# Kernel optimization log

Measured on AMD Instinct MI355X. Metric: run time of the kernel, lower is better.

## Reference

```python
import jax, jax.numpy as jnp
import numpy as np

N = 100000          # original nodes
E = 1600000         # edges (avg degree 16)
D_IN = 128
D_BLOOM = 16        # (bloom_lmax+1)^2 with lmax=3
D_OUT = 128
D_INTER = D_BLOOM + D_OUT
K = 4               # blooms per node
PF = 4              # pool factor (nodes per cluster)
C = N // PF         # coarsened nodes
MIN_RADIUS = 0.1


def setup_inputs() -> dict:
    key = jax.random.key(0)
    ks = jax.random.split(key, 10)
    x = jax.random.normal(ks[0], (N, D_IN), jnp.float32)
    pos = jax.random.normal(ks[1], (N, 3), jnp.float32)
    edge_index = jax.random.randint(ks[2], (2, E), 0, N)
    edge_attr = jax.random.normal(ks[3], (E, 3), jnp.float32)
    batch = jnp.sort(jax.random.randint(ks[4], (N,), 0, 64))
    # learned parameters (stand-ins for the injected submodules)
    W_conv = jax.random.normal(ks[5], (D_IN, D_INTER), jnp.float32) / np.sqrt(D_IN)
    W_edge = jax.random.normal(ks[6], (3, D_INTER), jnp.float32)
    D_bloom = jax.random.normal(ks[7], (K, D_BLOOM, 3), jnp.float32) / np.sqrt(D_BLOOM)
    W_gather = jax.random.normal(ks[8], (D_OUT, D_OUT), jnp.float32) / np.sqrt(D_OUT)
    W_gattr = jax.random.normal(ks[9], (3, D_OUT), jnp.float32)
    return dict(x=x, pos=pos, edge_index=edge_index, edge_attr=edge_attr, batch=batch,
                W_conv=W_conv, W_edge=W_edge, D_bloom=D_bloom,
                W_gather=W_gather, W_gattr=W_gattr)


def reference(x, pos, edge_index, edge_attr, batch, W_conv, W_edge, D_bloom, W_gather, W_gattr):
    src, dst = edge_index[0], edge_index[1]

    # ---- bloom conv: per-edge message, scatter-sum to destination nodes ----
    msg = x[src] @ W_conv + edge_attr @ W_edge           # [E, D_INTER]
    out = jax.ops.segment_sum(msg, dst, num_segments=N)  # [N, D_INTER]
    sph = out[:, :D_BLOOM]                               # [N, D_BLOOM]
    feat = out[:, D_BLOOM:]                              # [N, D_OUT]

    # ---- bloom: K candidate points per node ----
    offsets = MIN_RADIUS * jnp.tanh(jnp.einsum('nb,kbd->nkd', sph, D_bloom))  # [N,K,3]
    bloom_pos = (pos[:, None, :] + offsets).reshape(N * K, 3)
    bloom_batch = jnp.repeat(jnp.arange(N), K)           # bloom node -> original node

    # ---- cluster: deterministic pool_factor grouping ----
    clusters = bloom_batch // PF                         # [N*K] bloom -> cluster
    node_cluster = jnp.arange(N) // PF                   # [N] node -> cluster (coalesced pairs)

    # new_pos = scatter_mean(pos[coalesced node], cluster): exactly PF nodes per cluster
    new_pos = jax.ops.segment_sum(pos, node_cluster, num_segments=C) / PF  # [C,3]

    # ---- gather conv: bipartite message passing N features -> C clusters ----
    gather_edge_attr = pos[bloom_batch] - new_pos[clusters]                 # [N*K,3]
    gm = feat[bloom_batch] @ W_gather + gather_edge_attr @ W_gattr          # [N*K,D_OUT]
    x_new = jax.ops.segment_sum(gm, clusters, num_segments=C) / (K * PF)    # [C,D_OUT]

    # ---- new_edge_index: spspmm chain == map endpoints to clusters + coalesce ----
    enc = node_cluster[src] * C + node_cluster[dst]      # encode cluster pairs
    enc_u = jnp.unique(enc, size=E, fill_value=0)        # coalesced, padded with (0,0)
    new_edge_index = jnp.stack([enc_u // C, enc_u % C])  # [2, E] (padded)
    new_edge_attr = new_pos[new_edge_index[1]] - new_pos[new_edge_index[0]]

    # ---- new_batch: graph id of each cluster (batch is sorted per graph) ----
    new_batch = jax.ops.segment_max(batch, node_cluster, num_segments=C)

    return (x_new, new_pos, new_edge_index, new_edge_attr, new_batch)
```

## Files before the change

kernel.cpp:

```cpp
#include <hip/hip_runtime.h>
#include <hip/hip_bf16.h>
#include <stdint.h>

typedef unsigned int uint_t;
typedef unsigned short ushort_t;

#define NN 100000
#define EE 1600000
#define CC 25000
#define DINTER 144
#define NBKT 196
#define NBKT2 1568
#define NSEG 6272
#define KCAP 1024

#define W_M1B      0u
#define W_AGGB     8384u
#define W_PAGG     1658384u
#define W_PKA4     14858384u
#define W_PKC      21258384u
#define W_OFFS2    22858384u
#define W_BHA2     23058385u
#define W_BHC      23059953u
#define W_BBA2     23060149u
#define W_BCURA2   23061718u
#define W_BBC      23063286u
#define W_BCURC    23063483u
#define WS_WORDS   23066816u

#define O_XNEW  0u
#define O_POS   3200000u
#define O_EI    3275000u
#define O_ATTR  6475000u
#define O_BATCH 11275000u

static __device__ __forceinline__ uint_t f2bf(float f) {
    union { float f; uint_t i; } v; v.f = f;
    uint_t x = v.i;
    return (x + 0x7fffu + ((x >> 16) & 1u)) >> 16;
}
static __device__ __forceinline__ float bf2f(ushort_t u) {
    union { uint_t i; float f; } v; v.i = ((uint_t)u) << 16; return v.f;
}

__global__ void xpack(const float4* __restrict__ x4, uint2* __restrict__ xb2) {
    int i = blockIdx.x * 256 + threadIdx.x;
    if (i >= NN * 32) return;
    float4 v = x4[i];
    uint2 r;
    r.x = f2bf(v.x) | (f2bf(v.y) << 16);
    r.y = f2bf(v.z) | (f2bf(v.w) << 16);
    xb2[i] = r;
}

__global__ void build_m1f(const float* __restrict__ Wconv,
                          const float* __restrict__ Wedge,
                          const float* __restrict__ Wg,
                          ushort_t* __restrict__ m1b) {
    int j = blockIdx.x;
    int o = threadIdx.x;
    const float* wrow = (j < 128) ? (Wconv + j * DINTER + 16)
                                  : (Wedge + (j - 128) * DINTER + 16);
    float acc = 0.f;
    for (int f = 0; f < 128; ++f)
        acc += wrow[f] * Wg[f * 128 + o];
    m1b[j * 128 + o] = (ushort_t)f2bf(acc);
}

__global__ void edge_hist2(const int* __restrict__ ei,
                           uint_t* __restrict__ bhA2, uint_t* __restrict__ bhC) {
    __shared__ uint_t hA[NBKT2], hC[NBKT];
    int tid = threadIdx.x;
    for (int i = tid; i < NBKT2; i += 1024) hA[i] = 0;
    for (int i = tid; i < NBKT; i += 1024) hC[i] = 0;
    __syncthreads();
    for (int e = blockIdx.x * 1024 + tid; e < EE; e += 256 * 1024) {
        uint_t u = (uint_t)ei[e];
        uint_t v = (uint_t)ei[EE + e];
        atomicAdd(&hA[(u / 12500u) * 196u + (v >> 9)], 1u);
        atomicAdd(&hC[u >> 9], 1u);
    }
    __syncthreads();
    for (int i = tid; i < NBKT2; i += 1024) if (hA[i]) atomicAdd(&bhA2[i], hA[i]);
    for (int i = tid; i < NBKT; i += 1024)  if (hC[i]) atomicAdd(&bhC[i], hC[i]);
}

__global__ void scan_small(const uint_t* __restrict__ in, uint_t* __restrict__ out,
                           uint_t* __restrict__ out2, int n) {
    __shared__ uint_t part[256];
    int tid = threadIdx.x;
    int per = (n + 255) >> 8;
    int lo = tid * per;
    int hi = lo + per; if (hi > n) hi = n;
    if (lo > n) lo = n;
    uint_t s = 0;
    for (int i = lo; i < hi; ++i) s += in[i];
    part[tid] = s;
    __syncthreads();
    for (int off = 1; off < 256; off <<= 1) {
        uint_t v = (tid >= off) ? part[tid - off] : 0u;
        __syncthreads();
        part[tid] += v;
        __syncthreads();
    }
    uint_t run = part[tid] - s;
    for (int i = lo; i < hi; ++i) {
        out[i] = run;
        if (out2) out2[i] = run;
        run += in[i];
    }
    if (tid == 255) out[n] = run;
}

#define TPB 4096
__global__ void bucket_place_AC(const int* __restrict__ ei, const float* __restrict__ ea,
                                uint_t* __restrict__ bcurA, uint_t* __restrict__ bcurC,
                                uint4* __restrict__ pk4, uint_t* __restrict__ pkC) {
    __shared__ uint_t histA[NBKT2], gbaseA[NBKT2], curA[NBKT2];
    __shared__ uint_t pkst[TPB];
    __shared__ uint_t gpk[TPB];
    __shared__ uint_t histC[NBKT], lbaseC[NBKT], gbaseC[NBKT], curC[NBKT];
    __shared__ uint_t part[1024];
    int tid = threadIdx.x;
    int t0 = blockIdx.x * TPB;
    int nt = EE - t0; if (nt > TPB) nt = TPB;
    for (int i = tid; i < NBKT2; i += 1024) { histA[i] = 0; curA[i] = 0; }
    for (int i = tid; i < NBKT; i += 1024) { histC[i] = 0; curC[i] = 0; }
    __syncthreads();
    for (int i = tid; i < nt; i += 1024) {
        int e = t0 + i;
        uint_t u = (uint_t)ei[e];
        uint_t v = (uint_t)ei[EE + e];
        atomicAdd(&histA[(u / 12500u) * 196u + (v >> 9)], 1u);
        uint_t w = ((u >> 2) << 15) | (v >> 2);
        pkst[i] = w;
        atomicAdd(&histC[w >> 22], 1u);
    }
    __syncthreads();
    for (int b = tid; b < NBKT2; b += 1024) {
        uint_t h = histA[b];
        if (h) gbaseA[b] = atomicAdd(&bcurA[b], h);
    }
    uint_t h = (tid < NBKT) ? histC[tid] : 0u;
    if (tid < NBKT) gbaseC[tid] = atomicAdd(&bcurC[tid], h);
    part[tid] = h;
    __syncthreads();
    for (int off = 1; off < 1024; off <<= 1) {
        uint_t v = (tid >= off) ? part[tid - off] : 0u;
        __syncthreads();
        part[tid] += v;
        __syncthreads();
    }
    if (tid < NBKT) lbaseC[tid] = part[tid] - h;
    __syncthreads();
    for (int i = tid; i < nt; i += 1024) {
        uint_t w = pkst[i];
        uint_t b = w >> 22;
        uint_t r = lbaseC[b] + atomicAdd(&curC[b], 1u);
        gpk[r] = w;
    }
    __syncthreads();
    for (int r = tid; r < nt; r += 1024) {
        uint_t w = gpk[r];
        uint_t b = w >> 22;
        pkC[gbaseC[b] + ((uint_t)r - lbaseC[b])] = w;
    }
    for (int i = tid; i < nt; i += 1024) {
        int e = t0 + i;
        uint_t u = (uint_t)ei[e];
        uint_t v = (uint_t)ei[EE + e];
        uint_t b = (u / 12500u) * 196u + (v >> 9);
        uint_t r = gbaseA[b] + atomicAdd(&curA[b], 1u);
        uint4 p;
        p.x = (((v >> 2) & 127u) << 17) | u;
        p.y = __float_as_uint(ea[(size_t)e * 3 + 0]);
        p.z = __float_as_uint(ea[(size_t)e * 3 + 1]);
        p.w = __float_as_uint(ea[(size_t)e * 3 + 2]);
        pk4[r] = p;
    }
}

__global__ void bucket_sort_A2(const uint_t* __restrict__ bbA2, const uint4* __restrict__ pk4,
                               uint_t* __restrict__ pkW, uint_t* __restrict__ paggw,
                               uint_t* __restrict__ offs2) {
    __shared__ uint4 st[2048];
    __shared__ uint_t hist[128], base2[128], cur[128];
    __shared__ float eacc0[128], eacc1[128], eacc2[128];
    __shared__ uint_t part[256];
    int tid = threadIdx.x, bk = blockIdx.x;
    uint_t s = bbA2[bk], epos = bbA2[bk + 1];
    int n = (int)(epos - s);
    if (n > 2048) n = 2048;
    if (tid < 128) {
        hist[tid] = 0; cur[tid] = 0;
        eacc0[tid] = 0.f; eacc1[tid] = 0.f; eacc2[tid] = 0.f;
    }
    for (int i = tid; i < n; i += 256) st[i] = pk4[s + i];
    __syncthreads();
    for (int i = tid; i < n; i += 256) {
        uint4 p = st[i];
        uint_t d = p.x >> 17;
        atomicAdd(&hist[d], 1u);
        atomicAdd(&eacc0[d], __uint_as_float(p.y));
        atomicAdd(&eacc1[d], __uint_as_float(p.z));
        atomicAdd(&eacc2[d], __uint_as_float(p.w));
    }
    __syncthreads();
    uint_t h = (tid < 128) ? hist[tid] : 0u;
    part[tid] = h;
    __syncthreads();
    for (int off = 1; off < 256; off <<= 1) {
        uint_t v = (tid >= off) ? part[tid - off] : 0u;
        __syncthreads();
        part[tid] += v;
        __syncthreads();
    }
    int sl = bk / 196, q = bk - sl * 196;
    if (tid < 128) {
        base2[tid] = part[tid] - h;
        int c = q * 128 + tid;
        if (c < CC) {
            uint_t kk = (uint_t)sl * CC + (uint_t)c;
            offs2[kk] = s + base2[tid];
            paggw[(size_t)kk * 66 + 64] = f2bf(eacc0[tid]) | (f2bf(eacc1[tid]) << 16);
            paggw[(size_t)kk * 66 + 65] = f2bf(eacc2[tid]);
        }
    }
    if (bk == 0 && tid == 0) offs2[8 * CC] = EE;
    __syncthreads();
    for (int i = tid; i < n; i += 256) {
        uint4 p = st[i];
        uint_t d = p.x >> 17;
        uint_t r = base2[d] + atomicAdd(&cur[d], 1u);
        pkW[s + r] = p.x;
    }
}

__global__ void bucket_sort_C(const uint_t* __restrict__ bbC, uint_t* __restrict__ pkC,
                              uint_t* __restrict__ csub) {
    __shared__ uint_t st[8960];
    __shared__ uint_t hist[32], base2[32], cur[32];
    __shared__ uint_t part[256];
    int tid = threadIdx.x, bk = blockIdx.x;
    uint_t s = bbC[bk], epos = bbC[bk + 1];
    int n = (int)(epos - s);
    if (n > 8960) n = 8960;
    if (tid < 32) { hist[tid] = 0; cur[tid] = 0; }
    for (int i = tid; i < n; i += 256) st[i] = pkC[s + i];
    __syncthreads();
    for (int i = tid; i < n; i += 256) atomicAdd(&hist[(st[i] >> 17) & 31u], 1u);
    __syncthreads();
    uint_t h = (tid < 32) ? hist[tid] : 0u;
    part[tid] = h;
    __syncthreads();
    for (int off = 1; off < 256; off <<= 1) {
        uint_t v = (tid >= off) ? part[tid - off] : 0u;
        __syncthreads();
        part[tid] += v;
        __syncthreads();
    }
    if (tid < 32) {
        base2[tid] = part[tid] - h;
        csub[bk * 32 + tid] = s + base2[tid];
    }
    if (bk == 0 && tid == 0) csub[NSEG] = EE;
    __syncthreads();
    for (int i = tid; i < n; i += 256) {
        uint_t w = st[i];
        uint_t d = (w >> 17) & 31u;
        uint_t r = base2[d] + atomicAdd(&cur[d], 1u);
        pkC[s + r] = w;
    }
}

__global__ void cluster_pass(const float* __restrict__ pos, const int* __restrict__ batch,
                             float* __restrict__ out) {
    int c = blockIdx.x * 256 + threadIdx.x;
    if (c >= CC) return;
    float px = 0.f, py = 0.f, pz = 0.f;
    for (int j = 0; j < 4; ++j) {
        int n = c * 4 + j;
        px += pos[n * 3 + 0];
        py += pos[n * 3 + 1];
        pz += pos[n * 3 + 2];
    }
    px *= 0.25f; py *= 0.25f; pz *= 0.25f;
    out[O_POS + c * 3 + 0] = px;
    out[O_POS + c * 3 + 1] = py;
    out[O_POS + c * 3 + 2] = pz;
    int b = batch[c * 4];
    b = max(b, batch[c * 4 + 1]);
    b = max(b, batch[c * 4 + 2]);
    b = max(b, batch[c * 4 + 3]);
    out[O_BATCH + c] = (float)b;
}

#define CPW 8
__global__ void cluster_reduce5(const uint_t* __restrict__ offs2, const uint_t* __restrict__ pkW,
                                const uint_t* __restrict__ xb, uint_t* __restrict__ paggw) {
    int tid = threadIdx.x;
    int lane = tid & 63;
    int s = blockIdx.x & 7;
    int c0 = ((blockIdx.x >> 3) * 4 + (tid >> 6)) * CPW;
    if (c0 >= CC) return;
    uint_t kk0 = (uint_t)s * CC + (uint_t)c0;
    const uint_t* xl = xb + lane;
    for (int cl = 0; cl < CPW; ++cl) {
        if (c0 + cl >= CC) break;
        uint_t start = (uint_t)__builtin_amdgcn_readfirstlane((int)offs2[kk0 + cl]);
        uint_t end   = (uint_t)__builtin_amdgcn_readfirstlane((int)offs2[kk0 + cl + 1]);
        float a0 = 0.f, a1 = 0.f;
        uint_t i = start;
        for (; i + 4u <= end; i += 4u) {
            uint_t w0 = pkW[i + 0u];
            uint_t w1 = pkW[i + 1u];
            uint_t w2 = pkW[i + 2u];
            uint_t w3 = pkW[i + 3u];
            uint_t x0 = xl[(size_t)(w0 & 0x1FFFFu) * 64u];
            uint_t x1 = xl[(size_t)(w1 & 0x1FFFFu) * 64u];
            uint_t x2 = xl[(size_t)(w2 & 0x1FFFFu) * 64u];
            uint_t x3 = xl[(size_t)(w3 & 0x1FFFFu) * 64u];
            a0 += bf2f((ushort_t)(x0 & 0xffffu)); a1 += bf2f((ushort_t)(x0 >> 16));
            a0 += bf2f((ushort_t)(x1 & 0xffffu)); a1 += bf2f((ushort_t)(x1 >> 16));
            a0 += bf2f((ushort_t)(x2 & 0xffffu)); a1 += bf2f((ushort_t)(x2 >> 16));
            a0 += bf2f((ushort_t)(x3 & 0xffffu)); a1 += bf2f((ushort_t)(x3 >> 16));
        }
        for (; i < end; ++i) {
            uint_t wj = pkW[i];
            uint_t xv = xl[(size_t)(wj & 0x1FFFFu) * 64u];
            a0 += bf2f((ushort_t)(xv & 0xffffu));
            a1 += bf2f((ushort_t)(xv >> 16));
        }
        paggw[(size_t)(kk0 + (uint_t)cl) * 66 + lane] = f2bf(a0) | (f2bf(a1) << 16);
    }
}

#define GEMM_CPB 32
__global__ void gemm_tiled(const uint_t* __restrict__ paggw, const ushort_t* __restrict__ m1b,
                           float* __restrict__ out) {
    __shared__ ushort_t m1s[131 * 128];
    __shared__ __align__(16) float srowT[132][8];
    int tid = threadIdx.x;
    {
        const uint_t* m1w = (const uint_t*)m1b;
        uint_t* m1sw = (uint_t*)m1s;
        for (int i = tid; i < 131 * 64; i += 256) m1sw[i] = m1w[i];
    }
    int o = tid & 127, half = tid >> 7;
    int c0b = blockIdx.x * GEMM_CPB;
    for (int it = 0; it < GEMM_CPB / 8; ++it) {
        int c0 = c0b + it * 8;
        __syncthreads();
        for (int i = tid; i < 528; i += 256) {
            int cg = i / 66, rem = i - cg * 66;
            int c = c0 + cg;
            float lo = 0.f, hi = 0.f;
            if (c < CC) {
                #pragma unroll
                for (int s = 0; s < 8; ++s) {
                    uint_t w = paggw[((size_t)s * 25000u + (uint_t)c) * 66 + rem];
                    lo += bf2f((ushort_t)(w & 0xffffu));
                    hi += bf2f((ushort_t)(w >> 16));
                }
            }
            srowT[rem * 2][cg]     = lo;
            srowT[rem * 2 + 1][cg] = hi;
        }
        __syncthreads();
        float acc0 = 0.f, acc1 = 0.f, acc2 = 0.f, acc3 = 0.f;
        #pragma unroll 4
        for (int j = 0; j < 131; ++j) {
            float m = bf2f(m1s[j * 128 + o]);
            float4 s = *(const float4*)&srowT[j][half * 4];
            acc0 += s.x * m;
            acc1 += s.y * m;
            acc2 += s.z * m;
            acc3 += s.w * m;
        }
        int cb = c0 + half * 4;
        if (cb + 0 < CC) out[O_XNEW + (size_t)(cb + 0) * 128 + o] = 0.25f * acc0;
        if (cb + 1 < CC) out[O_XNEW + (size_t)(cb + 1) * 128 + o] = 0.25f * acc1;
        if (cb + 2 < CC) out[O_XNEW + (size_t)(cb + 2) * 128 + o] = 0.25f * acc2;
        if (cb + 3 < CC) out[O_XNEW + (size_t)(cb + 3) * 128 + o] = 0.25f * acc3;
    }
}

__global__ void enc_count(const uint_t* __restrict__ csub, const uint_t* __restrict__ pkC,
                          uint_t* __restrict__ bcnt, uint_t* __restrict__ kbuf) {
    __shared__ uint_t bmp[3125];
    __shared__ uint_t sh[256];
    int tid = threadIdx.x, bid = blockIdx.x;
    uint_t s = csub[bid], epos = csub[bid + 1];
    int n = (int)(epos - s);
    for (int i = tid; i < 3125; i += 256) bmp[i] = 0;
    __syncthreads();
    for (int i = tid; i < n; i += 256) {
        uint_t w = pkC[s + i];
        uint_t le = ((w >> 15) & 3u) * 25000u + (w & 32767u);
        atomicOr(&bmp[le >> 5], 1u << (le & 31u));
    }
    __syncthreads();
    int lo = tid * 13, hi = lo + 13;
    if (lo > 3125) lo = 3125;
    if (hi > 3125) hi = 3125;
    uint_t mine = 0;
    for (int i = lo; i < hi; ++i) mine += __popc(bmp[i]);
    sh[tid] = mine;
    __syncthreads();
    for (int off = 1; off < 256; off <<= 1) {
        uint_t v = (tid >= off) ? sh[tid - off] : 0u;
        __syncthreads();
        sh[tid] += v;
        __syncthreads();
    }
    uint_t r = sh[tid] - mine;
    uint_t kb = (uint_t)bid * KCAP;
    for (int i = lo; i < hi; ++i) {
        uint_t bits = bmp[i];
        while (bits) {
            int b = __builtin_ctz(bits);
            bits &= bits - 1u;
            if (r < KCAP) kbuf[kb + r] = (uint_t)i * 32u + (uint_t)b;
            r++;
        }
    }
    if (tid == 255) bcnt[bid] = min(sh[255], (uint_t)KCAP);
}

__global__ void tail_zero(const uint_t* __restrict__ ebase, float* __restrict__ out) {
    uint_t total = ebase[NSEG];
    uint_t idx = blockIdx.x * 256u + (uint_t)threadIdx.x;
    uint_t stride = gridDim.x * 256u;
    for (uint_t k = total + idx; k < EE; k += stride) {
        out[O_EI + k] = 0.f;
        out[O_EI + EE + k] = 0.f;
    }
    for (uint_t k = 3u * total + idx; k < 3u * EE; k += stride) {
        out[O_ATTR + k] = 0.f;
    }
}

__global__ void enc_emit(const uint_t* __restrict__ ebase, const uint_t* __restrict__ kbuf,
                         float* __restrict__ out) {
    int tid = threadIdx.x, bid = blockIdx.x;
    uint_t g0 = ebase[bid], g1 = ebase[bid + 1];
    int cnt = (int)(g1 - g0);
    const float* np = out + O_POS;
    uint_t ubase = ((uint_t)(bid >> 5)) * 128u + ((uint_t)(bid & 31)) * 4u;
    uint_t kb = (uint_t)bid * KCAP;
    for (int r = tid; r < cnt; r += 256) {
        uint_t le = kbuf[kb + r];
        uint_t uo = le / 25000u;
        uint_t v = le - uo * 25000u;
        uint_t u = ubase + uo;
        uint_t rank = g0 + (uint_t)r;
        out[O_EI + rank] = (float)u;
        out[O_EI + EE + rank] = (float)v;
        out[O_ATTR + (size_t)rank * 3 + 0] = np[v * 3 + 0] - np[u * 3 + 0];
        out[O_ATTR + (size_t)rank * 3 + 1] = np[v * 3 + 1] - np[u * 3 + 1];
        out[O_ATTR + (size_t)rank * 3 + 2] = np[v * 3 + 2] - np[u * 3 + 2];
    }
}

extern "C" void kernel_launch(void* const* d_in, const int* in_sizes, int n_in,
                              void* d_out, int out_size, void* d_ws, size_t ws_size,
                              hipStream_t stream) {
    const float* x     = (const float*)d_in[0];
    const float* pos   = (const float*)d_in[1];
    const int*   ei    = (const int*)d_in[2];
    const float* ea    = (const float*)d_in[3];
    const int*   batch = (const int*)d_in[4];
    const float* Wconv = (const float*)d_in[5];
    const float* Wedge = (const float*)d_in[6];
    const float* Wg    = (const float*)d_in[8];

    float*  out = (float*)d_out;
    uint_t* ws  = (uint_t*)d_ws;

    if (ws_size < (size_t)WS_WORDS * 4) return;

    ushort_t* m1b    = (ushort_t*)(ws + W_M1B);
    uint_t*   pkW    = ws + W_AGGB;
    uint_t*   paggw  = ws + W_PAGG;
    uint4*    pk4    = (uint4*)(ws + W_PKA4);
    uint_t*   pkC    = ws + W_PKC;
    uint_t*   offs2  = ws + W_OFFS2;
    uint_t*   bhA2   = ws + W_BHA2;
    uint_t*   bhC    = ws + W_BHC;
    uint_t*   bbA2   = ws + W_BBA2;
    uint_t*   bcurA2 = ws + W_BCURA2;
    uint_t*   bbC    = ws + W_BBC;
    uint_t*   bcurC  = ws + W_BCURC;
    uint_t*   xb     = (uint_t*)(out + O_EI);
    uint_t*   csub   = ws + W_PKA4;
    uint_t*   bcnt2  = ws + W_PKA4 + 8192u;
    uint_t*   ebase2 = ws + W_PKA4 + 16384u;
    uint_t*   kbuf   = ws + W_PAGG;

    hipMemsetAsync(bhA2, 0, (size_t)(NBKT2 + NBKT) * 4, stream);

    xpack<<<dim3(12500), dim3(256), 0, stream>>>((const float4*)x, (uint2*)xb);
    build_m1f<<<dim3(131), dim3(128), 0, stream>>>(Wconv, Wedge, Wg, m1b);
    edge_hist2<<<dim3(256), dim3(1024), 0, stream>>>(ei, bhA2, bhC);
    scan_small<<<dim3(1), dim3(256), 0, stream>>>(bhA2, bbA2, bcurA2, NBKT2);
    scan_small<<<dim3(1), dim3(256), 0, stream>>>(bhC, bbC, bcurC, NBKT);
    bucket_place_AC<<<dim3((EE + TPB - 1) / TPB), dim3(1024), 0, stream>>>(ei, ea, bcurA2, bcurC, pk4, pkC);
    bucket_sort_A2<<<dim3(NBKT2), dim3(256), 0, stream>>>(bbA2, pk4, pkW, paggw, offs2);
    cluster_pass<<<dim3(98), dim3(256), 0, stream>>>(pos, batch, out);
    cluster_reduce5<<<dim3(((CC + 4 * CPW - 1) / (4 * CPW)) * 8), dim3(256), 0, stream>>>(offs2, pkW, xb, paggw);
    gemm_tiled<<<dim3((CC + GEMM_CPB - 1) / GEMM_CPB), dim3(256), 0, stream>>>(paggw, m1b, out);
    bucket_sort_C<<<dim3(NBKT), dim3(256), 0, stream>>>(bbC, pkC, csub);
    enc_count<<<dim3(NSEG), dim3(256), 0, stream>>>(csub, pkC, bcnt2, kbuf);
    scan_small<<<dim3(1), dim3(256), 0, stream>>>(bcnt2, ebase2, (uint_t*)0, NSEG);
    tail_zero<<<dim3(512), dim3(256), 0, stream>>>(ebase2, out);
    enc_emit<<<dim3(NSEG), dim3(256), 0, stream>>>(ebase2, kbuf, out);
}
```

Measured before the change: 423.9 us.

## Split bucket placement across 8 slices per tile to cut shared memory

The bucket placement kernel now launches 8 blocks per 4096-edge tile, each handling only the edges whose source slice (or C-bucket modulo 8) matches its block index. This shrinks per-block shared arrays so more blocks fit per CU and the grid is 8x larger. The cost is that every edge index is read 8 times, and each slice is capped at CCAP entries, which can silently drop edges if a slice overflows. A no-op ternary was also added in bucket_sort_A2.

```diff
diff --git a/kernel.cpp b/kernel.cpp
--- a/kernel.cpp
+++ b/kernel.cpp
@@ -113,36 +113,49 @@
 }
 
 #define TPB 4096
+#define CCAP 1536
 __global__ void bucket_place_AC(const int* __restrict__ ei, const float* __restrict__ ea,
                                 uint_t* __restrict__ bcurA, uint_t* __restrict__ bcurC,
                                 uint4* __restrict__ pk4, uint_t* __restrict__ pkC) {
-    __shared__ uint_t histA[NBKT2], gbaseA[NBKT2], curA[NBKT2];
-    __shared__ uint_t pkst[TPB];
-    __shared__ uint_t gpk[TPB];
+    __shared__ uint_t histA[NBKT], gbaseA[NBKT], curA[NBKT];
     __shared__ uint_t histC[NBKT], lbaseC[NBKT], gbaseC[NBKT], curC[NBKT];
+    __shared__ uint_t pkst[CCAP];
+    __shared__ uint_t gpk[CCAP];
+    __shared__ uint2  ast[CCAP];
     __shared__ uint_t part[1024];
+    __shared__ uint_t nA, nC;
     int tid = threadIdx.x;
-    int t0 = blockIdx.x * TPB;
+    uint_t s = (uint_t)(blockIdx.x & 7);
+    int t0 = (blockIdx.x >> 3) * TPB;
     int nt = EE - t0; if (nt > TPB) nt = TPB;
-    for (int i = tid; i < NBKT2; i += 1024) { histA[i] = 0; curA[i] = 0; }
-    for (int i = tid; i < NBKT; i += 1024) { histC[i] = 0; curC[i] = 0; }
+    for (int i = tid; i < NBKT; i += 1024) { histA[i] = 0; curA[i] = 0; histC[i] = 0; curC[i] = 0; }
+    if (tid == 0) { nA = 0; nC = 0; }
     __syncthreads();
     for (int i = tid; i < nt; i += 1024) {
         int e = t0 + i;
         uint_t u = (uint_t)ei[e];
         uint_t v = (uint_t)ei[EE + e];
-        atomicAdd(&histA[(u / 12500u) * 196u + (v >> 9)], 1u);
-        uint_t w = ((u >> 2) << 15) | (v >> 2);
-        pkst[i] = w;
-        atomicAdd(&histC[w >> 22], 1u);
-    }
-    __syncthreads();
-    for (int b = tid; b < NBKT2; b += 1024) {
+        if (u / 12500u == s) {
+            uint_t q = v >> 9;
+            atomicAdd(&histA[q], 1u);
+            uint_t k = atomicAdd(&nA, 1u);
+            if (k < CCAP) { ast[k].x = (q << 24) | (((v >> 2) & 127u) << 17) | u; ast[k].y = (uint_t)e; }
+        }
+        uint_t cb = u >> 9;
+        if ((cb & 7u) == s) {
+            atomicAdd(&histC[cb], 1u);
+            uint_t k = atomicAdd(&nC, 1u);
+            if (k < CCAP) pkst[k] = ((u >> 2) << 15) | (v >> 2);
+        }
+    }
+    __syncthreads();
+    for (int b = tid; b < NBKT; b += 1024) {
         uint_t h = histA[b];
-        if (h) gbaseA[b] = atomicAdd(&bcurA[b], h);
+        if (h) gbaseA[b] = atomicAdd(&bcurA[s * 196u + (uint_t)b], h);
+        uint_t hc = histC[b];
+        if (hc) gbaseC[b] = atomicAdd(&bcurC[b], hc);
     }
     uint_t h = (tid < NBKT) ? histC[tid] : 0u;
-    if (tid < NBKT) gbaseC[tid] = atomicAdd(&bcurC[tid], h);
     part[tid] = h;
     __syncthreads();
     for (int off = 1; off < 1024; off <<= 1) {
@@ -153,29 +166,29 @@
     }
     if (tid < NBKT) lbaseC[tid] = part[tid] - h;
     __syncthreads();
-    for (int i = tid; i < nt; i += 1024) {
-        uint_t w = pkst[i];
+    uint_t mC = nC; if (mC > CCAP) mC = CCAP;
+    uint_t mA = nA; if (mA > CCAP) mA = CCAP;
+    for (uint_t k = tid; k < mC; k += 1024u) {
+        uint_t w = pkst[k];
         uint_t b = w >> 22;
         uint_t r = lbaseC[b] + atomicAdd(&curC[b], 1u);
         gpk[r] = w;
     }
     __syncthreads();
-    for (int r = tid; r < nt; r += 1024) {
+    for (uint_t r = tid; r < mC; r += 1024u) {
         uint_t w = gpk[r];
         uint_t b = w >> 22;
-        pkC[gbaseC[b] + ((uint_t)r - lbaseC[b])] = w;
-    }
-    for (int i = tid; i < nt; i += 1024) {
-        int e = t0 + i;
-        uint_t u = (uint_t)ei[e];
-        uint_t v = (uint_t)ei[EE + e];
-        uint_t b = (u / 12500u) * 196u + (v >> 9);
-        uint_t r = gbaseA[b] + atomicAdd(&curA[b], 1u);
+        pkC[gbaseC[b] + (r - lbaseC[b])] = w;
+    }
+    for (uint_t k = tid; k < mA; k += 1024u) {
+        uint2 a = ast[k];
+        uint_t q = a.x >> 24;
+        uint_t r = gbaseA[q] + atomicAdd(&curA[q], 1u);
         uint4 p;
-        p.x = (((v >> 2) & 127u) << 17) | u;
-        p.y = __float_as_uint(ea[(size_t)e * 3 + 0]);
-        p.z = __float_as_uint(ea[(size_t)e * 3 + 1]);
-        p.w = __float_as_uint(ea[(size_t)e * 3 + 2]);
+        p.x = a.x & 0xFFFFFFu;
+        p.y = __float_as_uint(ea[(size_t)a.y * 3 + 0]);
+        p.z = __float_as_uint(ea[(size_t)a.y * 3 + 1]);
+        p.w = __float_as_uint(ea[(size_t)a.y * 3 + 2]);
         pk4[r] = p;
     }
 }
@@ -232,7 +245,7 @@
         uint4 p = st[i];
         uint_t d = p.x >> 17;
         uint_t r = base2[d] + atomicAdd(&cur[d], 1u);
-        pkW[s + r] = p.x;
+        pkW[s + r] = p.x & 0x1FFFFu ? p.x : p.x;
     }
 }
 
@@ -504,7 +517,7 @@
     edge_hist2<<<dim3(256), dim3(1024), 0, stream>>>(ei, bhA2, bhC);
     scan_small<<<dim3(1), dim3(256), 0, stream>>>(bhA2, bbA2, bcurA2, NBKT2);
     scan_small<<<dim3(1), dim3(256), 0, stream>>>(bhC, bbC, bcurC, NBKT);
-    bucket_place_AC<<<dim3((EE + TPB - 1) / TPB), dim3(1024), 0, stream>>>(ei, ea, bcurA2, bcurC, pk4, pkC);
+    bucket_place_AC<<<dim3(((EE + TPB - 1) / TPB) * 8), dim3(1024), 0, stream>>>(ei, ea, bcurA2, bcurC, pk4, pkC);
     bucket_sort_A2<<<dim3(NBKT2), dim3(256), 0, stream>>>(bbA2, pk4, pkW, paggw, offs2);
     cluster_pass<<<dim3(98), dim3(256), 0, stream>>>(pos, batch, out);
     cluster_reduce5<<<dim3(((CC + 4 * CPW - 1) / (4 * CPW)) * 8), dim3(256), 0, stream>>>(offs2, pkW, xb, paggw);
```

Measured after the change: 457.2 us. 1.08x slower.
